# Optimization experiments

Measured on AMD Instinct MI355X. Metric: run time of the kernel, lower is better.

The kernel has to match this reference:

```python
import jax, jax.numpy as jnp
import numpy as np

E = 8      # num_experts
K = 2      # top-k
DIM = 1024
DFF = 2048  # fused gate+up width; intermediate = DFF // 2 == DIM


def setup_inputs() -> dict:
    key = jax.random.key(0)
    ks = jax.random.split(key, 5)
    B, S = 4, 2048
    x = jax.random.normal(ks[0], (B, S, DIM), dtype=jnp.float32)
    Wg = jax.random.normal(ks[1], (E, DIM), dtype=jnp.float32) * 0.02
    bg = jax.random.normal(ks[2], (E,), dtype=jnp.float32) * 0.02
    w1 = jax.random.normal(ks[3], (E, DFF, DIM), dtype=jnp.float32) * 0.02
    w2 = jax.random.normal(ks[4], (E, DIM, DFF // 2), dtype=jnp.float32) * 0.02
    return {"x": x, "Wg": Wg, "bg": bg, "w1": w1, "w2": w2}


def _moe(x, Wg, bg, w1, w2):
    B, S, D = x.shape
    t = x.reshape(-1, D)                      # [T, D] tokens
    logits = t @ Wg.T + bg                    # [T, E]
    probs = jax.nn.softmax(logits, axis=-1)
    topw, topi = jax.lax.top_k(probs, K)      # [T, K]
    topw = topw / jnp.sum(topw, axis=-1, keepdims=True)  # renormalize=True
    # per-token combine weight for each expert (0 if not selected): [T, E]
    combine = jnp.sum(jax.nn.one_hot(topi, E, dtype=t.dtype) * topw[..., None], axis=1)

    def body(acc, packed):
        w1e, w2e, ce = packed                 # [DFF, D], [D, DFF//2], [T]
        h = t @ w1e.T                         # [T, DFF]
        gate, up = jnp.split(h, 2, axis=-1)   # silu_and_mul (SwiGLU)
        a = jax.nn.silu(gate) * up            # [T, DFF//2]
        o = a @ w2e.T                         # [T, D]
        return acc + ce[:, None] * o, None

    out, _ = jax.lax.scan(body, jnp.zeros_like(t), (w1, w2, combine.T))
    return out.reshape(B, S, D)


def reference(x, Wg, bg, w1, w2):
    return _moe(x, Wg, bg, w1, w2)
```

## Files before the change

kernel.cpp:

```cpp
#include <hip/hip_runtime.h>
#include <hip/hip_bf16.h>
#include <cstdint>

#define T_TOKENS 8192
#define DIM 1024
#define NEXP 8
#define DFFH 1024
#define ROWCAP 17408
#define NCHUNK 16
#define MAXMT 24

typedef __attribute__((ext_vector_type(8))) short bf16x8;
typedef __attribute__((ext_vector_type(4))) float f32x4;

__device__ __forceinline__ ushort f2bf(float f) {
  uint32_t u = __float_as_uint(f);
  uint32_t r = (u + 0x7fffu + ((u >> 16) & 1u)) >> 16;
  return (ushort)r;
}
__device__ __forceinline__ float bf2f(ushort u) {
  return __uint_as_float(((uint32_t)u) << 16);
}

__device__ __forceinline__ void async16(const void* g, const void* l) {
  __builtin_amdgcn_global_load_lds(
      (const __attribute__((address_space(1))) void*)(uintptr_t)g,
      (__attribute__((address_space(3))) void*)(uintptr_t)l, 16, 0, 0);
}

__global__ __launch_bounds__(256) void cast_kernel(
    const float4* __restrict__ w1, const float4* __restrict__ w2,
    ushort* __restrict__ w1b, ushort* __restrict__ w2b) {
  const int NW1 = NEXP * 2048 * DIM / 4;
  const int NW2 = NEXP * DIM * DFFH / 4;
  const int total = NW1 + NW2;
  for (int i = blockIdx.x * 256 + threadIdx.x; i < total; i += 2048 * 256) {
    float4 v; ushort* dst;
    if (i < NW1) { v = w1[i]; dst = w1b + (size_t)i * 4; }
    else { int j = i - NW1; v = w2[j]; dst = w2b + (size_t)j * 4; }
    ushort4 o4;
    o4.x = f2bf(v.x); o4.y = f2bf(v.y); o4.z = f2bf(v.z); o4.w = f2bf(v.w);
    *(ushort4*)dst = o4;
  }
}

__global__ __launch_bounds__(256) void gate_kernel(
    const float4* __restrict__ x4, const float4* __restrict__ Wg4,
    const float* __restrict__ bg, int* __restrict__ top2e,
    float2* __restrict__ top2w, ushort* __restrict__ xb) {
  __shared__ float4 wgl[NEXP * 256];
  const int tid = threadIdx.x;
  for (int i = tid; i < NEXP * 256; i += 256) wgl[i] = Wg4[i];
  __syncthreads();
  const int wave = tid >> 6, lane = tid & 63;
  const float bgsel = bg[lane & 7];
  const int t0 = (blockIdx.x * 4 + wave) * 16;
  for (int tt = 0; tt < 16; ++tt) {
    const int t = t0 + tt;
    const float4* xr = x4 + (size_t)t * 256;
    ushort4* xw = (ushort4*)(xb + (size_t)t * DIM);
    float acc[NEXP];
#pragma unroll
    for (int e = 0; e < NEXP; ++e) acc[e] = 0.f;
#pragma unroll
    for (int j = 0; j < 4; ++j) {
      float4 xv = xr[lane + j * 64];
      ushort4 o4;
      o4.x = f2bf(xv.x); o4.y = f2bf(xv.y); o4.z = f2bf(xv.z); o4.w = f2bf(xv.w);
      xw[lane + j * 64] = o4;
#pragma unroll
      for (int e = 0; e < NEXP; ++e) {
        float4 wv = wgl[e * 256 + lane + j * 64];
        acc[e] += xv.x * wv.x + xv.y * wv.y + xv.z * wv.z + xv.w * wv.w;
      }
    }
#pragma unroll
    for (int e = 0; e < NEXP; ++e) {
      float v = acc[e];
      v += __shfl_xor(v, 1); v += __shfl_xor(v, 2); v += __shfl_xor(v, 4);
      acc[e] = v;
    }
    float v = acc[0];
#pragma unroll
    for (int e = 1; e < NEXP; ++e) v = ((lane & 7) == e) ? acc[e] : v;
    v += __shfl_xor(v, 8); v += __shfl_xor(v, 16); v += __shfl_xor(v, 32);
    v += bgsel;
    float m1 = v;
    m1 = fmaxf(m1, __shfl_xor(m1, 1));
    m1 = fmaxf(m1, __shfl_xor(m1, 2));
    m1 = fmaxf(m1, __shfl_xor(m1, 4));
    unsigned long long mk = __ballot(v == m1);
    int bi = (int)(__ffsll(mk) - 1) & 7;
    float v2 = (((lane & 7) == bi) ? -1e30f : v);
    float m2 = v2;
    m2 = fmaxf(m2, __shfl_xor(m2, 1));
    m2 = fmaxf(m2, __shfl_xor(m2, 2));
    m2 = fmaxf(m2, __shfl_xor(m2, 4));
    mk = __ballot(v2 == m2);
    int si = (int)(__ffsll(mk) - 1) & 7;
    if (lane == 0) {
      float w0 = 1.f / (1.f + __expf(m2 - m1));
      top2e[t] = bi | (si << 8);
      top2w[t] = make_float2(w0, 1.f - w0);
    }
  }
}

__global__ __launch_bounds__(1024) void route_kernel(
    const int* __restrict__ top2e, int* __restrict__ cnt,
    int* __restrict__ off, int* __restrict__ base ) {
  __shared__ int chunkcnt[NCHUNK][NEXP];
  const int tid = threadIdx.x;
  int c[NEXP];
#pragma unroll
  for (int e = 0; e < NEXP; ++e) c[e] = 0;
  const int4* p = (const int4*)(top2e + tid * 8);
  int4 a = p[0], b = p[1];
  int vals[8] = {a.x, a.y, a.z, a.w, b.x, b.y, b.z, b.w};
#pragma unroll
  for (int k = 0; k < 8; ++k) {
    int e0 = vals[k] & 255, e1 = (vals[k] >> 8) & 255;
#pragma unroll
    for (int e = 0; e < NEXP; ++e) c[e] += (e0 == e) + (e1 == e);
  }
#pragma unroll
  for (int e = 0; e < NEXP; ++e) {
    c[e] += __shfl_xor(c[e], 1);  c[e] += __shfl_xor(c[e], 2);
    c[e] += __shfl_xor(c[e], 4);  c[e] += __shfl_xor(c[e], 8);
    c[e] += __shfl_xor(c[e], 16); c[e] += __shfl_xor(c[e], 32);
  }
  const int wave = tid >> 6, lane = tid & 63;
  if (lane == 0) {
#pragma unroll
    for (int e = 0; e < NEXP; ++e) chunkcnt[wave][e] = c[e];
  }
  __syncthreads();
  if (tid == 0) {
    int o = 0;
    off[0] = 0;
    for (int e = 0; e < NEXP; ++e) {
      int tot = 0;
      for (int w = 0; w < NCHUNK; ++w) tot += chunkcnt[w][e];
      cnt[e] = tot;
      int run = o;
      for (int w = 0; w < NCHUNK; ++w) { base[w * NEXP + e] = run; run += chunkcnt[w][e]; }
      o += (tot + 127) & ~127;
      off[e + 1] = o;
    }
  }
}

__global__ __launch_bounds__(512) void scatter_kernel(
    const int* __restrict__ top2e, const float2* __restrict__ top2w,
    const int* __restrict__ base, int* __restrict__ rows_token,
    float* __restrict__ rows_weight, int2* __restrict__ tok2row) {
  __shared__ int lcnt[NEXP];
  const int tid = threadIdx.x;
  if (tid < NEXP) lcnt[tid] = 0;
  __syncthreads();
  const int b = blockIdx.x;
  const int t = b * 512 + tid;
  int pk = top2e[t];
  float2 w = top2w[t];
  int e0 = pk & 255, e1 = (pk >> 8) & 255;
  int p0 = atomicAdd(&lcnt[e0], 1);
  int p1 = atomicAdd(&lcnt[e1], 1);
  int r0 = base[b * NEXP + e0] + p0;
  int r1 = base[b * NEXP + e1] + p1;
  rows_token[r0] = t; rows_weight[r0] = w.x;
  rows_token[r1] = t; rows_weight[r1] = w.y;
  tok2row[t] = make_int2(r0, r1);
}

__global__ __launch_bounds__(256) void mlpA_kernel(
    const ushort* __restrict__ xb, const ushort* __restrict__ w1b,
    const int* __restrict__ rows_token, const int* __restrict__ cnt,
    const int* __restrict__ off, ushort* __restrict__ abuf) {
  const int bid = blockIdx.x;
  const int e = bid & 7;
  const int pos = bid >> 3;
  const int mt = pos >> 4, nt = pos & 15;
  const int count = cnt[e];
  if (mt * 128 >= count) return;
  const int base = off[e];

  __shared__ ushort As[2][128 * 64];
  __shared__ ushort Bs[2][2][64 * 64];

  const int tid = threadIdx.x;
  const int wave = tid >> 6, lane = tid & 63;
  const int wm = wave >> 1, wn = wave & 1;
  const int cg = tid & 7;
  const int r7w = (tid >> 3) & 7;
  const int cgs = (cg ^ r7w) * 8;

  const ushort* gA[4];
#pragma unroll
  for (int i = 0; i < 4; ++i) {
    int row = i * 32 + (tid >> 3);
    int r = mt * 128 + row;
    int tok = (r < count) ? rows_token[base + r] : 0;
    gA[i] = xb + ((size_t)tok * DIM + cgs);
  }
  const ushort* gBg[2];
  const ushort* gBu[2];
#pragma unroll
  for (int i = 0; i < 2; ++i) {
    int row = i * 32 + (tid >> 3);
    gBg[i] = w1b + ((size_t)(e * 2048 + nt * 64 + row) * DIM + cgs);
    gBu[i] = w1b + ((size_t)(e * 2048 + 1024 + nt * 64 + row) * DIM + cgs);
  }

#define STAGE_A1(b_, k0_)                                             \
  {                                                                   \
    _Pragma("unroll")                                                 \
    for (int i = 0; i < 4; ++i)                                       \
      async16(gA[i] + (k0_), &As[b_][(i * 256 + wave * 64) * 8]);     \
    _Pragma("unroll")                                                 \
    for (int i = 0; i < 2; ++i) {                                     \
      async16(gBg[i] + (k0_), &Bs[b_][0][(i * 256 + wave * 64) * 8]); \
      async16(gBu[i] + (k0_), &Bs[b_][1][(i * 256 + wave * 64) * 8]); \
    }                                                                 \
  }

  const f32x4 zero = {0.f, 0.f, 0.f, 0.f};
  f32x4 accg[4][2], accu[4][2];
#pragma unroll
  for (int m = 0; m < 4; ++m)
#pragma unroll
    for (int n = 0; n < 2; ++n) { accg[m][n] = zero; accu[m][n] = zero; }

  const int xr = (lane & 7) << 3;

  STAGE_A1(0, 0);
  __syncthreads();

  for (int t = 0; t < 16; ++t) {
    const int b = t & 1;
    if (t < 15) STAGE_A1(b ^ 1, (t + 1) * 64);
#pragma unroll
    for (int kk = 0; kk < 2; ++kk) {
      const int ko = (kk * 32 + (lane >> 4) * 8) ^ xr;
      bf16x8 af[4];
#pragma unroll
      for (int m = 0; m < 4; ++m)
        af[m] = *(const bf16x8*)&As[b][(wm * 64 + m * 16 + (lane & 15)) * 64 + ko];
#pragma unroll
      for (int n = 0; n < 2; ++n) {
        bf16x8 bgf = *(const bf16x8*)&Bs[b][0][(wn * 32 + n * 16 + (lane & 15)) * 64 + ko];
        bf16x8 buf_ = *(const bf16x8*)&Bs[b][1][(wn * 32 + n * 16 + (lane & 15)) * 64 + ko];
#pragma unroll
        for (int m = 0; m < 4; ++m) {
          accg[m][n] = __builtin_amdgcn_mfma_f32_16x16x32_bf16(af[m], bgf, accg[m][n], 0, 0, 0);
          accu[m][n] = __builtin_amdgcn_mfma_f32_16x16x32_bf16(af[m], buf_, accu[m][n], 0, 0, 0);
        }
      }
    }
    __syncthreads();
  }

  const size_t arow0 = (size_t)(base + mt * 128 + wm * 64);
#pragma unroll
  for (int m = 0; m < 4; ++m)
#pragma unroll
    for (int n = 0; n < 2; ++n)
#pragma unroll
      for (int r = 0; r < 4; ++r) {
        float g = accg[m][n][r], u = accu[m][n][r];
        float a = (g / (1.f + __expf(-g))) * u;
        size_t row = arow0 + m * 16 + (lane >> 4) * 4 + r;
        int col = nt * 64 + wn * 32 + n * 16 + (lane & 15);
        abuf[row * DFFH + col] = f2bf(a);
      }
}

__global__ __launch_bounds__(256) void mlpB_kernel(
    const ushort* __restrict__ abuf, const ushort* __restrict__ w2b,
    const float* __restrict__ rows_weight, const int* __restrict__ cnt,
    const int* __restrict__ off, ushort* __restrict__ obuf) {
  const int bid = blockIdx.x;
  const int e = bid & 7;
  const int pos = bid >> 3;
  const int mt = pos >> 4, nt = pos & 15;
  const int count = cnt[e];
  if (mt * 128 >= count) return;
  const int base = off[e];

  __shared__ ushort As[2][128 * 64];
  __shared__ ushort Bs[2][64 * 64];

  const int tid = threadIdx.x;
  const int wave = tid >> 6, lane = tid & 63;
  const int wm = wave >> 1, wn = wave & 1;
  const int cg = tid & 7;
  const int r7w = (tid >> 3) & 7;
  const int cgs = (cg ^ r7w) * 8;

  const ushort* gA[4];
#pragma unroll
  for (int i = 0; i < 4; ++i) {
    int row = i * 32 + (tid >> 3);
    gA[i] = abuf + ((size_t)(base + mt * 128 + row) * DFFH + cgs);
  }
  const ushort* gB[2];
#pragma unroll
  for (int i = 0; i < 2; ++i) {
    int row = i * 32 + (tid >> 3);
    gB[i] = w2b + ((size_t)(e * 1024 + nt * 64 + row) * DFFH + cgs);
  }

#define STAGE_B1(b_, k0_)                                           \
  {                                                                 \
    _Pragma("unroll")                                               \
    for (int i = 0; i < 4; ++i)                                     \
      async16(gA[i] + (k0_), &As[b_][(i * 256 + wave * 64) * 8]);   \
    _Pragma("unroll")                                               \
    for (int i = 0; i < 2; ++i)                                     \
      async16(gB[i] + (k0_), &Bs[b_][(i * 256 + wave * 64) * 8]);   \
  }

  const f32x4 zero = {0.f, 0.f, 0.f, 0.f};
  f32x4 acc[4][2];
#pragma unroll
  for (int m = 0; m < 4; ++m)
#pragma unroll
    for (int n = 0; n < 2; ++n) acc[m][n] = zero;

  const int xr = (lane & 7) << 3;

  STAGE_B1(0, 0);
  __syncthreads();

  for (int t = 0; t < 16; ++t) {
    const int b = t & 1;
    if (t < 15) STAGE_B1(b ^ 1, (t + 1) * 64);
#pragma unroll
    for (int kk = 0; kk < 2; ++kk) {
      const int ko = (kk * 32 + (lane >> 4) * 8) ^ xr;
      bf16x8 af[4];
#pragma unroll
      for (int m = 0; m < 4; ++m)
        af[m] = *(const bf16x8*)&As[b][(wm * 64 + m * 16 + (lane & 15)) * 64 + ko];
#pragma unroll
      for (int n = 0; n < 2; ++n) {
        bf16x8 bf_ = *(const bf16x8*)&Bs[b][(wn * 32 + n * 16 + (lane & 15)) * 64 + ko];
#pragma unroll
        for (int m = 0; m < 4; ++m)
          acc[m][n] = __builtin_amdgcn_mfma_f32_16x16x32_bf16(af[m], bf_, acc[m][n], 0, 0, 0);
      }
    }
    __syncthreads();
  }

#pragma unroll
  for (int m = 0; m < 4; ++m) {
#pragma unroll
    for (int r = 0; r < 4; ++r) {
      int lrow = mt * 128 + wm * 64 + m * 16 + (lane >> 4) * 4 + r;
      if (lrow < count) {
        float wgt = rows_weight[base + lrow];
#pragma unroll
        for (int n = 0; n < 2; ++n) {
          int col = nt * 64 + wn * 32 + n * 16 + (lane & 15);
          obuf[(size_t)(base + lrow) * DIM + col] = f2bf(wgt * acc[m][n][r]);
        }
      }
    }
  }
}

__global__ __launch_bounds__(256) void combine_kernel(
    const ushort* __restrict__ obuf, const int2* __restrict__ tok2row,
    float* __restrict__ out) {
  const int t = blockIdx.x;
  int2 rr = tok2row[t];
  const ushort4* p0 = (const ushort4*)(obuf + (size_t)rr.x * DIM);
  const ushort4* p1 = (const ushort4*)(obuf + (size_t)rr.y * DIM);
  float4* po = (float4*)(out + (size_t)t * DIM);
  const int c = threadIdx.x;
  ushort4 a = p0[c], b = p1[c];
  float4 o;
  o.x = bf2f(a.x) + bf2f(b.x);
  o.y = bf2f(a.y) + bf2f(b.y);
  o.z = bf2f(a.z) + bf2f(b.z);
  o.w = bf2f(a.w) + bf2f(b.w);
  po[c] = o;
}

extern "C" void kernel_launch(void* const* d_in, const int* in_sizes, int n_in,
                              void* d_out, int out_size, void* d_ws, size_t ws_size,
                              hipStream_t stream) {
  const float* x = (const float*)d_in[0];
  const float* Wg = (const float*)d_in[1];
  const float* bg = (const float*)d_in[2];
  const float* w1 = (const float*)d_in[3];
  const float* w2 = (const float*)d_in[4];
  float* out = (float*)d_out;

  char* ws = (char*)d_ws;
  ushort* xb = (ushort*)ws;
  ushort* w1b = xb + (size_t)T_TOKENS * DIM;
  ushort* w2b = w1b + (size_t)NEXP * 2048 * DIM;
  ushort* abuf = w2b + (size_t)NEXP * DIM * DFFH;
  char* p = (char*)(abuf + (size_t)ROWCAP * DFFH);
  int* top2e = (int*)p;            p += T_TOKENS * 4;
  float2* top2w = (float2*)p;      p += T_TOKENS * 8;
  int* rows_token = (int*)p;       p += ROWCAP * 4;
  float* rows_weight = (float*)p;  p += ROWCAP * 4;
  int2* tok2row = (int2*)p;        p += T_TOKENS * 8;
  int* cnt = (int*)p;              p += 32;
  int* off = (int*)p;              p += 64;
  int* base = (int*)p;             p += NCHUNK * NEXP * 4;
  ushort* obuf = xb;

  cast_kernel<<<2048, 256, 0, stream>>>((const float4*)w1, (const float4*)w2,
                                        w1b, w2b);
  gate_kernel<<<128, 256, 0, stream>>>((const float4*)x, (const float4*)Wg, bg,
                                       top2e, top2w, xb);
  route_kernel<<<1, 1024, 0, stream>>>(top2e, cnt, off, base);
  scatter_kernel<<<NCHUNK, 512, 0, stream>>>(top2e, top2w, base, rows_token,
                                             rows_weight, tok2row);
  mlpA_kernel<<<8 * MAXMT * 16, 256, 0, stream>>>(xb, w1b, rows_token, cnt, off, abuf);
  mlpB_kernel<<<8 * MAXMT * 16, 256, 0, stream>>>(abuf, w2b, rows_weight, cnt, off, obuf);
  combine_kernel<<<T_TOKENS, 256, 0, stream>>>(obuf, tok2row, out);
}
```

Measured before the change: 244.2 us.

## Switch MoE GEMMs to 32x32x16 MFMA and widen mlpB N-tile to 128

Both expert GEMM kernels move from 16x16x32 bf16 MFMA tiles to 32x32x16 tiles with f32x16 accumulators. This cuts LDS fragment loads per MFMA and the instruction count. The main loop is unrolled into an explicit two-buffer ping-pong. mlpB also doubles its N tile to 128 columns, halving the grid and improving A-tile reuse, at the cost of more LDS per block. The epilogue index mapping is rewritten for the 32x32 accumulator layout, which risks layout mistakes, and the stores are narrower per lane.

```diff
diff --git a/kernel.cpp b/kernel.cpp
--- a/kernel.cpp
+++ b/kernel.cpp
@@ -12,6 +12,7 @@
 
 typedef __attribute__((ext_vector_type(8))) short bf16x8;
 typedef __attribute__((ext_vector_type(4))) float f32x4;
+typedef __attribute__((ext_vector_type(16))) float f32x16;
 
 __device__ __forceinline__ ushort f2bf(float f) {
   uint32_t u = __float_as_uint(f);
@@ -223,55 +224,58 @@
     }                                                                 \
   }
 
-  const f32x4 zero = {0.f, 0.f, 0.f, 0.f};
-  f32x4 accg[4][2], accu[4][2];
-#pragma unroll
-  for (int m = 0; m < 4; ++m)
-#pragma unroll
-    for (int n = 0; n < 2; ++n) { accg[m][n] = zero; accu[m][n] = zero; }
+  f32x16 accg0 = {0,0,0,0,0,0,0,0,0,0,0,0,0,0,0,0};
+  f32x16 accg1 = accg0, accu0 = accg0, accu1 = accg0;
 
   const int xr = (lane & 7) << 3;
+  const int la31 = lane & 31;
+  const int kbase = (lane >> 5) * 8;
+
+#define COMPA(b_)                                                              \
+  {                                                                            \
+    _Pragma("unroll")                                                          \
+    for (int kk = 0; kk < 4; ++kk) {                                           \
+      const int ko = (kk * 16 + kbase) ^ xr;                                   \
+      bf16x8 a0 = *(const bf16x8*)&As[b_][(wm * 64 + la31) * 64 + ko];         \
+      bf16x8 a1 = *(const bf16x8*)&As[b_][(wm * 64 + 32 + la31) * 64 + ko];    \
+      bf16x8 bg_ = *(const bf16x8*)&Bs[b_][0][(wn * 32 + la31) * 64 + ko];     \
+      bf16x8 bu_ = *(const bf16x8*)&Bs[b_][1][(wn * 32 + la31) * 64 + ko];     \
+      accg0 = __builtin_amdgcn_mfma_f32_32x32x16_bf16(a0, bg_, accg0, 0, 0, 0);\
+      accg1 = __builtin_amdgcn_mfma_f32_32x32x16_bf16(a1, bg_, accg1, 0, 0, 0);\
+      accu0 = __builtin_amdgcn_mfma_f32_32x32x16_bf16(a0, bu_, accu0, 0, 0, 0);\
+      accu1 = __builtin_amdgcn_mfma_f32_32x32x16_bf16(a1, bu_, accu1, 0, 0, 0);\
+    }                                                                          \
+  }
 
   STAGE_A1(0, 0);
   __syncthreads();
-
-  for (int t = 0; t < 16; ++t) {
-    const int b = t & 1;
-    if (t < 15) STAGE_A1(b ^ 1, (t + 1) * 64);
-#pragma unroll
-    for (int kk = 0; kk < 2; ++kk) {
-      const int ko = (kk * 32 + (lane >> 4) * 8) ^ xr;
-      bf16x8 af[4];
-#pragma unroll
-      for (int m = 0; m < 4; ++m)
-        af[m] = *(const bf16x8*)&As[b][(wm * 64 + m * 16 + (lane & 15)) * 64 + ko];
-#pragma unroll
-      for (int n = 0; n < 2; ++n) {
-        bf16x8 bgf = *(const bf16x8*)&Bs[b][0][(wn * 32 + n * 16 + (lane & 15)) * 64 + ko];
-        bf16x8 buf_ = *(const bf16x8*)&Bs[b][1][(wn * 32 + n * 16 + (lane & 15)) * 64 + ko];
-#pragma unroll
-        for (int m = 0; m < 4; ++m) {
-          accg[m][n] = __builtin_amdgcn_mfma_f32_16x16x32_bf16(af[m], bgf, accg[m][n], 0, 0, 0);
-          accu[m][n] = __builtin_amdgcn_mfma_f32_16x16x32_bf16(af[m], buf_, accu[m][n], 0, 0, 0);
-        }
-      }
-    }
+#pragma unroll
+  for (int it = 0; it < 8; ++it) {
+    STAGE_A1(1, it * 128 + 64);
+    COMPA(0);
     __syncthreads();
-  }
-
-  const size_t arow0 = (size_t)(base + mt * 128 + wm * 64);
-#pragma unroll
-  for (int m = 0; m < 4; ++m)
-#pragma unroll
-    for (int n = 0; n < 2; ++n)
-#pragma unroll
-      for (int r = 0; r < 4; ++r) {
-        float g = accg[m][n][r], u = accu[m][n][r];
-        float a = (g / (1.f + __expf(-g))) * u;
-        size_t row = arow0 + m * 16 + (lane >> 4) * 4 + r;
-        int col = nt * 64 + wn * 32 + n * 16 + (lane & 15);
-        abuf[row * DFFH + col] = f2bf(a);
-      }
+    if (it < 7) STAGE_A1(0, it * 128 + 128);
+    COMPA(1);
+    __syncthreads();
+  }
+
+  const int colg = nt * 64 + wn * 32 + la31;
+  const size_t rbase = (size_t)(base + mt * 128 + wm * 64);
+  const int rlo = 4 * (lane >> 5);
+#pragma unroll
+  for (int s = 0; s < 2; ++s) {
+    const f32x16 g16 = s ? accg1 : accg0;
+    const f32x16 u16 = s ? accu1 : accu0;
+#pragma unroll
+    for (int r = 0; r < 16; ++r) {
+      int rr = (r & 3) + 8 * (r >> 2) + rlo;
+      float g = g16[r], u = u16[r];
+      float a = (g / (1.f + __expf(-g))) * u;
+      abuf[(rbase + s * 32 + rr) * DFFH + colg] = f2bf(a);
+    }
+  }
+#undef STAGE_A1
+#undef COMPA
 }
 
 __global__ __launch_bounds__(256) void mlpB_kernel(
@@ -281,13 +285,13 @@
   const int bid = blockIdx.x;
   const int e = bid & 7;
   const int pos = bid >> 3;
-  const int mt = pos >> 4, nt = pos & 15;
+  const int mt = pos >> 3, nt = pos & 7;
   const int count = cnt[e];
   if (mt * 128 >= count) return;
   const int base = off[e];
 
   __shared__ ushort As[2][128 * 64];
-  __shared__ ushort Bs[2][64 * 64];
+  __shared__ ushort Bs[2][128 * 64];
 
   const int tid = threadIdx.x;
   const int wave = tid >> 6, lane = tid & 63;
@@ -302,71 +306,76 @@
     int row = i * 32 + (tid >> 3);
     gA[i] = abuf + ((size_t)(base + mt * 128 + row) * DFFH + cgs);
   }
-  const ushort* gB[2];
-#pragma unroll
-  for (int i = 0; i < 2; ++i) {
+  const ushort* gB[4];
+#pragma unroll
+  for (int i = 0; i < 4; ++i) {
     int row = i * 32 + (tid >> 3);
-    gB[i] = w2b + ((size_t)(e * 1024 + nt * 64 + row) * DFFH + cgs);
+    gB[i] = w2b + ((size_t)(e * 1024 + nt * 128 + row) * DFFH + cgs);
   }
 
 #define STAGE_B1(b_, k0_)                                           \
   {                                                                 \
     _Pragma("unroll")                                               \
-    for (int i = 0; i < 4; ++i)                                     \
+    for (int i = 0; i < 4; ++i) {                                   \
       async16(gA[i] + (k0_), &As[b_][(i * 256 + wave * 64) * 8]);   \
-    _Pragma("unroll")                                               \
-    for (int i = 0; i < 2; ++i)                                     \
       async16(gB[i] + (k0_), &Bs[b_][(i * 256 + wave * 64) * 8]);   \
-  }
-
-  const f32x4 zero = {0.f, 0.f, 0.f, 0.f};
-  f32x4 acc[4][2];
-#pragma unroll
-  for (int m = 0; m < 4; ++m)
-#pragma unroll
-    for (int n = 0; n < 2; ++n) acc[m][n] = zero;
+    }                                                               \
+  }
+
+  f32x16 acc00 = {0,0,0,0,0,0,0,0,0,0,0,0,0,0,0,0};
+  f32x16 acc01 = acc00, acc10 = acc00, acc11 = acc00;
 
   const int xr = (lane & 7) << 3;
+  const int la31 = lane & 31;
+  const int kbase = (lane >> 5) * 8;
+
+#define COMPB(b_)                                                              \
+  {                                                                            \
+    _Pragma("unroll")                                                          \
+    for (int kk = 0; kk < 4; ++kk) {                                           \
+      const int ko = (kk * 16 + kbase) ^ xr;                                   \
+      bf16x8 a0 = *(const bf16x8*)&As[b_][(wm * 64 + la31) * 64 + ko];         \
+      bf16x8 a1 = *(const bf16x8*)&As[b_][(wm * 64 + 32 + la31) * 64 + ko];    \
+      bf16x8 b0 = *(const bf16x8*)&Bs[b_][(wn * 64 + la31) * 64 + ko];         \
+      bf16x8 b1 = *(const bf16x8*)&Bs[b_][(wn * 64 + 32 + la31) * 64 + ko];    \
+      acc00 = __builtin_amdgcn_mfma_f32_32x32x16_bf16(a0, b0, acc00, 0, 0, 0); \
+      acc01 = __builtin_amdgcn_mfma_f32_32x32x16_bf16(a0, b1, acc01, 0, 0, 0); \
+      acc10 = __builtin_amdgcn_mfma_f32_32x32x16_bf16(a1, b0, acc10, 0, 0, 0); \
+      acc11 = __builtin_amdgcn_mfma_f32_32x32x16_bf16(a1, b1, acc11, 0, 0, 0); \
+    }                                                                          \
+  }
 
   STAGE_B1(0, 0);
   __syncthreads();
-
-  for (int t = 0; t < 16; ++t) {
-    const int b = t & 1;
-    if (t < 15) STAGE_B1(b ^ 1, (t + 1) * 64);
-#pragma unroll
-    for (int kk = 0; kk < 2; ++kk) {
-      const int ko = (kk * 32 + (lane >> 4) * 8) ^ xr;
-      bf16x8 af[4];
-#pragma unroll
-      for (int m = 0; m < 4; ++m)
-        af[m] = *(const bf16x8*)&As[b][(wm * 64 + m * 16 + (lane & 15)) * 64 + ko];
-#pragma unroll
-      for (int n = 0; n < 2; ++n) {
-        bf16x8 bf_ = *(const bf16x8*)&Bs[b][(wn * 32 + n * 16 + (lane & 15)) * 64 + ko];
-#pragma unroll
-        for (int m = 0; m < 4; ++m)
-          acc[m][n] = __builtin_amdgcn_mfma_f32_16x16x32_bf16(af[m], bf_, acc[m][n], 0, 0, 0);
-      }
-    }
+#pragma unroll
+  for (int it = 0; it < 8; ++it) {
+    STAGE_B1(1, it * 128 + 64);
+    COMPB(0);
     __syncthreads();
-  }
-
-#pragma unroll
-  for (int m = 0; m < 4; ++m) {
-#pragma unroll
-    for (int r = 0; r < 4; ++r) {
-      int lrow = mt * 128 + wm * 64 + m * 16 + (lane >> 4) * 4 + r;
+    if (it < 7) STAGE_B1(0, it * 128 + 128);
+    COMPB(1);
+    __syncthreads();
+  }
+
+  const int rlo = 4 * (lane >> 5);
+  const int colb = nt * 128 + wn * 64 + la31;
+#pragma unroll
+  for (int s = 0; s < 2; ++s) {
+    const f32x16 c0 = s ? acc10 : acc00;
+    const f32x16 c1 = s ? acc11 : acc01;
+#pragma unroll
+    for (int r = 0; r < 16; ++r) {
+      int rr = (r & 3) + 8 * (r >> 2) + rlo;
+      int lrow = mt * 128 + wm * 64 + s * 32 + rr;
       if (lrow < count) {
         float wgt = rows_weight[base + lrow];
-#pragma unroll
-        for (int n = 0; n < 2; ++n) {
-          int col = nt * 64 + wn * 32 + n * 16 + (lane & 15);
-          obuf[(size_t)(base + lrow) * DIM + col] = f2bf(wgt * acc[m][n][r]);
-        }
+        obuf[(size_t)(base + lrow) * DIM + colb] = f2bf(wgt * c0[r]);
+        obuf[(size_t)(base + lrow) * DIM + colb + 32] = f2bf(wgt * c1[r]);
       }
     }
   }
+#undef STAGE_B1
+#undef COMPB
 }
 
 __global__ __launch_bounds__(256) void combine_kernel(
@@ -421,6 +430,6 @@
   scatter_kernel<<<NCHUNK, 512, 0, stream>>>(top2e, top2w, base, rows_token,
                                              rows_weight, tok2row);
   mlpA_kernel<<<8 * MAXMT * 16, 256, 0, stream>>>(xb, w1b, rows_token, cnt, off, abuf);
-  mlpB_kernel<<<8 * MAXMT * 16, 256, 0, stream>>>(abuf, w2b, rows_weight, cnt, off, obuf);
+  mlpB_kernel<<<8 * MAXMT * 8, 256, 0, stream>>>(abuf, w2b, rows_weight, cnt, off, obuf);
   combine_kernel<<<T_TOKENS, 256, 0, stream>>>(obuf, tok2row, out);
 }
```

Measured after the change: 250.5 us. 1.03x slower.

## Enlarge MoE GEMM tiles to 256-row blocks with 32x32 MFMA and 512 threads

Applied to the files above, without the earlier changes.

Both expert GEMM kernels move to 512-thread blocks with 256-row M tiles and larger N tiles (128 gate+up columns for the first GEMM, 256 for the second), using 32x32x16 bf16 MFMA instead of 16x16x32. K steps of 32 are double-buffered through a new swizzled LDS layout. The aim is more data reuse per LDS load and fewer blocks re-reading weights. In exchange each thread holds more accumulator registers, and partially filled 256-row tiles waste more padded compute.

```diff
diff --git a/kernel.cpp b/kernel.cpp
--- a/kernel.cpp
+++ b/kernel.cpp
@@ -8,10 +8,10 @@
 #define DFFH 1024
 #define ROWCAP 17408
 #define NCHUNK 16
-#define MAXMT 24
+#define MAXMT 12
 
 typedef __attribute__((ext_vector_type(8))) short bf16x8;
-typedef __attribute__((ext_vector_type(4))) float f32x4;
+typedef __attribute__((ext_vector_type(16))) float f32x16;
 
 __device__ __forceinline__ ushort f2bf(float f) {
   uint32_t u = __float_as_uint(f);
@@ -172,201 +172,219 @@
   tok2row[t] = make_int2(r0, r1);
 }
 
-__global__ __launch_bounds__(256) void mlpA_kernel(
+__global__ __launch_bounds__(512, 2) void mlpA_kernel(
     const ushort* __restrict__ xb, const ushort* __restrict__ w1b,
     const int* __restrict__ rows_token, const int* __restrict__ cnt,
     const int* __restrict__ off, ushort* __restrict__ abuf) {
   const int bid = blockIdx.x;
   const int e = bid & 7;
   const int pos = bid >> 3;
-  const int mt = pos >> 4, nt = pos & 15;
+  const int mt = pos >> 3, nt = pos & 7;
   const int count = cnt[e];
-  if (mt * 128 >= count) return;
+  if (mt * 256 >= count) return;
   const int base = off[e];
-
-  __shared__ ushort As[2][128 * 64];
-  __shared__ ushort Bs[2][2][64 * 64];
+  const int padcnt = off[e + 1] - base;
+
+  __shared__ ushort As[2][8192];
+  __shared__ ushort Bs[2][8192];
 
   const int tid = threadIdx.x;
   const int wave = tid >> 6, lane = tid & 63;
-  const int wm = wave >> 1, wn = wave & 1;
-  const int cg = tid & 7;
-  const int r7w = (tid >> 3) & 7;
-  const int cgs = (cg ^ r7w) * 8;
-
-  const ushort* gA[4];
-#pragma unroll
-  for (int i = 0; i < 4; ++i) {
-    int row = i * 32 + (tid >> 3);
-    int r = mt * 128 + row;
+  const int wm = wave >> 2, wn = wave & 3;
+
+  const int sg = tid & 7, ln = tid >> 3;
+  const int gx = sg ^ (ln & 7);
+  const int ssub = (gx >> 2) & 1, skg = gx & 3;
+
+  const ushort* sA[2]; const ushort* sB[2];
+#pragma unroll
+  for (int i = 0; i < 2; ++i) {
+    int r = mt * 256 + ssub * 128 + i * 64 + ln;
     int tok = (r < count) ? rows_token[base + r] : 0;
-    gA[i] = xb + ((size_t)tok * DIM + cgs);
-  }
-  const ushort* gBg[2];
-  const ushort* gBu[2];
-#pragma unroll
-  for (int i = 0; i < 2; ++i) {
-    int row = i * 32 + (tid >> 3);
-    gBg[i] = w1b + ((size_t)(e * 2048 + nt * 64 + row) * DIM + cgs);
-    gBu[i] = w1b + ((size_t)(e * 2048 + 1024 + nt * 64 + row) * DIM + cgs);
-  }
-
-#define STAGE_A1(b_, k0_)                                             \
-  {                                                                   \
-    _Pragma("unroll")                                                 \
-    for (int i = 0; i < 4; ++i)                                       \
-      async16(gA[i] + (k0_), &As[b_][(i * 256 + wave * 64) * 8]);     \
-    _Pragma("unroll")                                                 \
-    for (int i = 0; i < 2; ++i) {                                     \
-      async16(gBg[i] + (k0_), &Bs[b_][0][(i * 256 + wave * 64) * 8]); \
-      async16(gBu[i] + (k0_), &Bs[b_][1][(i * 256 + wave * 64) * 8]); \
-    }                                                                 \
-  }
-
-  const f32x4 zero = {0.f, 0.f, 0.f, 0.f};
-  f32x4 accg[4][2], accu[4][2];
-#pragma unroll
-  for (int m = 0; m < 4; ++m)
-#pragma unroll
-    for (int n = 0; n < 2; ++n) { accg[m][n] = zero; accu[m][n] = zero; }
-
-  const int xr = (lane & 7) << 3;
-
-  STAGE_A1(0, 0);
+    sA[i] = xb + (size_t)tok * DIM + skg * 8;
+    sB[i] = w1b + (size_t)(e * 2048 + ssub * 1024 + nt * 128 + i * 64 + ln) * DIM + skg * 8;
+  }
+
+#define STG_A(b_, k0_)                                        \
+  {                                                           \
+    _Pragma("unroll")                                         \
+    for (int i = 0; i < 2; ++i) {                             \
+      async16(sA[i] + (k0_), &As[b_][(i * 512 + tid) * 8]);   \
+      async16(sB[i] + (k0_), &Bs[b_][(i * 512 + tid) * 8]);   \
+    }                                                         \
+  }
+
+  const f32x16 zz = {0,0,0,0,0,0,0,0,0,0,0,0,0,0,0,0};
+  f32x16 ag[4] = {zz, zz, zz, zz};
+  f32x16 au[4] = {zz, zz, zz, zz};
+
+  const int la31 = lane & 31, hi = lane >> 5, k7 = la31 & 7;
+  int gac[2], gbg[2], gbu[2];
+#pragma unroll
+  for (int ks = 0; ks < 2; ++ks) {
+    gac[ks] = ((wm * 4 + ks * 2 + hi) ^ k7) * 8;
+    gbg[ks] = ((ks * 2 + hi) ^ k7) * 8;
+    gbu[ks] = ((4 + ks * 2 + hi) ^ k7) * 8;
+  }
+  const int lbA = la31 * 64;
+  const int lbB = (wn * 32 + la31) * 64;
+
+#define CMP_A(b_)                                                                 \
+  {                                                                               \
+    _Pragma("unroll")                                                             \
+    for (int ks = 0; ks < 2; ++ks) {                                              \
+      bf16x8 a0 = *(const bf16x8*)&As[b_][lbA + gac[ks]];                         \
+      bf16x8 a1 = *(const bf16x8*)&As[b_][lbA + 2048 + gac[ks]];                  \
+      bf16x8 a2 = *(const bf16x8*)&As[b_][lbA + 4096 + gac[ks]];                  \
+      bf16x8 a3 = *(const bf16x8*)&As[b_][lbA + 6144 + gac[ks]];                  \
+      bf16x8 bg_ = *(const bf16x8*)&Bs[b_][lbB + gbg[ks]];                        \
+      bf16x8 bu_ = *(const bf16x8*)&Bs[b_][lbB + gbu[ks]];                        \
+      ag[0] = __builtin_amdgcn_mfma_f32_32x32x16_bf16(a0, bg_, ag[0], 0, 0, 0);   \
+      ag[1] = __builtin_amdgcn_mfma_f32_32x32x16_bf16(a1, bg_, ag[1], 0, 0, 0);   \
+      ag[2] = __builtin_amdgcn_mfma_f32_32x32x16_bf16(a2, bg_, ag[2], 0, 0, 0);   \
+      ag[3] = __builtin_amdgcn_mfma_f32_32x32x16_bf16(a3, bg_, ag[3], 0, 0, 0);   \
+      au[0] = __builtin_amdgcn_mfma_f32_32x32x16_bf16(a0, bu_, au[0], 0, 0, 0);   \
+      au[1] = __builtin_amdgcn_mfma_f32_32x32x16_bf16(a1, bu_, au[1], 0, 0, 0);   \
+      au[2] = __builtin_amdgcn_mfma_f32_32x32x16_bf16(a2, bu_, au[2], 0, 0, 0);   \
+      au[3] = __builtin_amdgcn_mfma_f32_32x32x16_bf16(a3, bu_, au[3], 0, 0, 0);   \
+    }                                                                             \
+  }
+
+  STG_A(0, 0);
   __syncthreads();
-
-  for (int t = 0; t < 16; ++t) {
-    const int b = t & 1;
-    if (t < 15) STAGE_A1(b ^ 1, (t + 1) * 64);
-#pragma unroll
-    for (int kk = 0; kk < 2; ++kk) {
-      const int ko = (kk * 32 + (lane >> 4) * 8) ^ xr;
-      bf16x8 af[4];
-#pragma unroll
-      for (int m = 0; m < 4; ++m)
-        af[m] = *(const bf16x8*)&As[b][(wm * 64 + m * 16 + (lane & 15)) * 64 + ko];
-#pragma unroll
-      for (int n = 0; n < 2; ++n) {
-        bf16x8 bgf = *(const bf16x8*)&Bs[b][0][(wn * 32 + n * 16 + (lane & 15)) * 64 + ko];
-        bf16x8 buf_ = *(const bf16x8*)&Bs[b][1][(wn * 32 + n * 16 + (lane & 15)) * 64 + ko];
-#pragma unroll
-        for (int m = 0; m < 4; ++m) {
-          accg[m][n] = __builtin_amdgcn_mfma_f32_16x16x32_bf16(af[m], bgf, accg[m][n], 0, 0, 0);
-          accu[m][n] = __builtin_amdgcn_mfma_f32_16x16x32_bf16(af[m], buf_, accu[m][n], 0, 0, 0);
-        }
+#pragma unroll
+  for (int it = 0; it < 16; ++it) {
+    STG_A(1, it * 64 + 32);
+    CMP_A(0);
+    __syncthreads();
+    if (it < 15) STG_A(0, it * 64 + 64);
+    CMP_A(1);
+    __syncthreads();
+  }
+
+  const int acol = nt * 128 + wn * 32 + la31;
+#pragma unroll
+  for (int m = 0; m < 4; ++m) {
+#pragma unroll
+    for (int r = 0; r < 16; ++r) {
+      int rr = (r & 3) + 8 * (r >> 2) + 4 * hi;
+      int row = mt * 256 + wm * 128 + m * 32 + rr;
+      if (row < padcnt) {
+        float g = ag[m][r], u = au[m][r];
+        float a = (g / (1.f + __expf(-g))) * u;
+        abuf[(size_t)(base + row) * DFFH + acol] = f2bf(a);
       }
     }
-    __syncthreads();
-  }
-
-  const size_t arow0 = (size_t)(base + mt * 128 + wm * 64);
-#pragma unroll
-  for (int m = 0; m < 4; ++m)
-#pragma unroll
-    for (int n = 0; n < 2; ++n)
-#pragma unroll
-      for (int r = 0; r < 4; ++r) {
-        float g = accg[m][n][r], u = accu[m][n][r];
-        float a = (g / (1.f + __expf(-g))) * u;
-        size_t row = arow0 + m * 16 + (lane >> 4) * 4 + r;
-        int col = nt * 64 + wn * 32 + n * 16 + (lane & 15);
-        abuf[row * DFFH + col] = f2bf(a);
-      }
-}
-
-__global__ __launch_bounds__(256) void mlpB_kernel(
+  }
+#undef STG_A
+#undef CMP_A
+}
+
+__global__ __launch_bounds__(512, 2) void mlpB_kernel(
     const ushort* __restrict__ abuf, const ushort* __restrict__ w2b,
     const float* __restrict__ rows_weight, const int* __restrict__ cnt,
     const int* __restrict__ off, ushort* __restrict__ obuf) {
   const int bid = blockIdx.x;
   const int e = bid & 7;
   const int pos = bid >> 3;
-  const int mt = pos >> 4, nt = pos & 15;
+  const int mt = pos >> 2, nt = pos & 3;
   const int count = cnt[e];
-  if (mt * 128 >= count) return;
+  if (mt * 256 >= count) return;
   const int base = off[e];
-
-  __shared__ ushort As[2][128 * 64];
-  __shared__ ushort Bs[2][64 * 64];
+  const int totrows = off[NEXP];
+
+  __shared__ ushort As[2][8192];
+  __shared__ ushort Bs[2][8192];
 
   const int tid = threadIdx.x;
   const int wave = tid >> 6, lane = tid & 63;
-  const int wm = wave >> 1, wn = wave & 1;
-  const int cg = tid & 7;
-  const int r7w = (tid >> 3) & 7;
-  const int cgs = (cg ^ r7w) * 8;
-
-  const ushort* gA[4];
-#pragma unroll
-  for (int i = 0; i < 4; ++i) {
-    int row = i * 32 + (tid >> 3);
-    gA[i] = abuf + ((size_t)(base + mt * 128 + row) * DFFH + cgs);
-  }
-  const ushort* gB[2];
+  const int wm = wave >> 2, wn = wave & 3;
+
+  const int sg = tid & 7, ln = tid >> 3;
+  const int gx = sg ^ (ln & 7);
+  const int ssub = (gx >> 2) & 1, skg = gx & 3;
+
+  const ushort* sA[2]; const ushort* sB[2];
 #pragma unroll
   for (int i = 0; i < 2; ++i) {
-    int row = i * 32 + (tid >> 3);
-    gB[i] = w2b + ((size_t)(e * 1024 + nt * 64 + row) * DFFH + cgs);
-  }
-
-#define STAGE_B1(b_, k0_)                                           \
-  {                                                                 \
-    _Pragma("unroll")                                               \
-    for (int i = 0; i < 4; ++i)                                     \
-      async16(gA[i] + (k0_), &As[b_][(i * 256 + wave * 64) * 8]);   \
-    _Pragma("unroll")                                               \
-    for (int i = 0; i < 2; ++i)                                     \
-      async16(gB[i] + (k0_), &Bs[b_][(i * 256 + wave * 64) * 8]);   \
-  }
-
-  const f32x4 zero = {0.f, 0.f, 0.f, 0.f};
-  f32x4 acc[4][2];
-#pragma unroll
-  for (int m = 0; m < 4; ++m)
-#pragma unroll
-    for (int n = 0; n < 2; ++n) acc[m][n] = zero;
-
-  const int xr = (lane & 7) << 3;
-
-  STAGE_B1(0, 0);
+    int ridx = base + mt * 256 + ssub * 128 + i * 64 + ln;
+    if (ridx > totrows - 1) ridx = totrows - 1;
+    sA[i] = abuf + (size_t)ridx * DFFH + skg * 8;
+    sB[i] = w2b + (size_t)(e * 1024 + nt * 256 + ssub * 128 + i * 64 + ln) * DFFH + skg * 8;
+  }
+
+#define STG_B(b_, k0_)                                        \
+  {                                                           \
+    _Pragma("unroll")                                         \
+    for (int i = 0; i < 2; ++i) {                             \
+      async16(sA[i] + (k0_), &As[b_][(i * 512 + tid) * 8]);   \
+      async16(sB[i] + (k0_), &Bs[b_][(i * 512 + tid) * 8]);   \
+    }                                                         \
+  }
+
+  const f32x16 zz = {0,0,0,0,0,0,0,0,0,0,0,0,0,0,0,0};
+  f32x16 c0[4] = {zz, zz, zz, zz};
+  f32x16 c1[4] = {zz, zz, zz, zz};
+
+  const int la31 = lane & 31, hi = lane >> 5, k7 = la31 & 7;
+  int gac[2], gbb[2];
+#pragma unroll
+  for (int ks = 0; ks < 2; ++ks) {
+    gac[ks] = ((wm * 4 + ks * 2 + hi) ^ k7) * 8;
+    gbb[ks] = (((wn >> 1) * 4 + ks * 2 + hi) ^ k7) * 8;
+  }
+  const int lbA = la31 * 64;
+  const int lbB = ((wn & 1) * 64 + la31) * 64;
+
+#define CMP_B(b_)                                                                 \
+  {                                                                               \
+    _Pragma("unroll")                                                             \
+    for (int ks = 0; ks < 2; ++ks) {                                              \
+      bf16x8 a0 = *(const bf16x8*)&As[b_][lbA + gac[ks]];                         \
+      bf16x8 a1 = *(const bf16x8*)&As[b_][lbA + 2048 + gac[ks]];                  \
+      bf16x8 a2 = *(const bf16x8*)&As[b_][lbA + 4096 + gac[ks]];                  \
+      bf16x8 a3 = *(const bf16x8*)&As[b_][lbA + 6144 + gac[ks]];                  \
+      bf16x8 b0 = *(const bf16x8*)&Bs[b_][lbB + gbb[ks]];                         \
+      bf16x8 b1 = *(const bf16x8*)&Bs[b_][lbB + 2048 + gbb[ks]];                  \
+      c0[0] = __builtin_amdgcn_mfma_f32_32x32x16_bf16(a0, b0, c0[0], 0, 0, 0);    \
+      c0[1] = __builtin_amdgcn_mfma_f32_32x32x16_bf16(a1, b0, c0[1], 0, 0, 0);    \
+      c0[2] = __builtin_amdgcn_mfma_f32_32x32x16_bf16(a2, b0, c0[2], 0, 0, 0);    \
+      c0[3] = __builtin_amdgcn_mfma_f32_32x32x16_bf16(a3, b0, c0[3], 0, 0, 0);    \
+      c1[0] = __builtin_amdgcn_mfma_f32_32x32x16_bf16(a0, b1, c1[0], 0, 0, 0);    \
+      c1[1] = __builtin_amdgcn_mfma_f32_32x32x16_bf16(a1, b1, c1[1], 0, 0, 0);    \
+      c1[2] = __builtin_amdgcn_mfma_f32_32x32x16_bf16(a2, b1, c1[2], 0, 0, 0);    \
+      c1[3] = __builtin_amdgcn_mfma_f32_32x32x16_bf16(a3, b1, c1[3], 0, 0, 0);    \
+    }                                                                             \
+  }
+
+  STG_B(0, 0);
   __syncthreads();
-
-  for (int t = 0; t < 16; ++t) {
-    const int b = t & 1;
-    if (t < 15) STAGE_B1(b ^ 1, (t + 1) * 64);
-#pragma unroll
-    for (int kk = 0; kk < 2; ++kk) {
-      const int ko = (kk * 32 + (lane >> 4) * 8) ^ xr;
-      bf16x8 af[4];
-#pragma unroll
-      for (int m = 0; m < 4; ++m)
-        af[m] = *(const bf16x8*)&As[b][(wm * 64 + m * 16 + (lane & 15)) * 64 + ko];
-#pragma unroll
-      for (int n = 0; n < 2; ++n) {
-        bf16x8 bf_ = *(const bf16x8*)&Bs[b][(wn * 32 + n * 16 + (lane & 15)) * 64 + ko];
-#pragma unroll
-        for (int m = 0; m < 4; ++m)
-          acc[m][n] = __builtin_amdgcn_mfma_f32_16x16x32_bf16(af[m], bf_, acc[m][n], 0, 0, 0);
+#pragma unroll
+  for (int it = 0; it < 16; ++it) {
+    STG_B(1, it * 64 + 32);
+    CMP_B(0);
+    __syncthreads();
+    if (it < 15) STG_B(0, it * 64 + 64);
+    CMP_B(1);
+    __syncthreads();
+  }
+
+  const int colb = nt * 256 + wn * 64 + la31;
+#pragma unroll
+  for (int m = 0; m < 4; ++m) {
+#pragma unroll
+    for (int r = 0; r < 16; ++r) {
+      int rr = (r & 3) + 8 * (r >> 2) + 4 * hi;
+      int row = mt * 256 + wm * 128 + m * 32 + rr;
+      if (row < count) {
+        float wgt = rows_weight[base + row];
+        obuf[(size_t)(base + row) * DIM + colb] = f2bf(wgt * c0[m][r]);
+        obuf[(size_t)(base + row) * DIM + colb + 32] = f2bf(wgt * c1[m][r]);
       }
     }
-    __syncthreads();
-  }
-
-#pragma unroll
-  for (int m = 0; m < 4; ++m) {
-#pragma unroll
-    for (int r = 0; r < 4; ++r) {
-      int lrow = mt * 128 + wm * 64 + m * 16 + (lane >> 4) * 4 + r;
-      if (lrow < count) {
-        float wgt = rows_weight[base + lrow];
-#pragma unroll
-        for (int n = 0; n < 2; ++n) {
-          int col = nt * 64 + wn * 32 + n * 16 + (lane & 15);
-          obuf[(size_t)(base + lrow) * DIM + col] = f2bf(wgt * acc[m][n][r]);
-        }
-      }
-    }
-  }
+  }
+#undef STG_B
+#undef CMP_B
 }
 
 __global__ __launch_bounds__(256) void combine_kernel(
@@ -420,7 +438,7 @@
   route_kernel<<<1, 1024, 0, stream>>>(top2e, cnt, off, base);
   scatter_kernel<<<NCHUNK, 512, 0, stream>>>(top2e, top2w, base, rows_token,
                                              rows_weight, tok2row);
-  mlpA_kernel<<<8 * MAXMT * 16, 256, 0, stream>>>(xb, w1b, rows_token, cnt, off, abuf);
-  mlpB_kernel<<<8 * MAXMT * 16, 256, 0, stream>>>(abuf, w2b, rows_weight, cnt, off, obuf);
+  mlpA_kernel<<<8 * MAXMT * 8, 512, 0, stream>>>(xb, w1b, rows_token, cnt, off, abuf);
+  mlpB_kernel<<<8 * MAXMT * 4, 512, 0, stream>>>(abuf, w2b, rows_weight, cnt, off, obuf);
   combine_kernel<<<T_TOKENS, 256, 0, stream>>>(obuf, tok2row, out);
 }
```

Measured after the change: 291.8 us. 19.5% more time.
